# Performance work log

Measured on AMD Instinct MI355X. Metric: run time of the kernel, lower is better.

Reference implementation:

```python
import jax, jax.numpy as jnp
import numpy as np

N_U, N_I, E = 100000, 200000, 500000
CH, H, HD, L, OUT, B_SEED = 128, 4, 32, 2, 64, 1024
NEG_SLOPE = 0.2
LN_EPS = 1e-5


def setup_inputs() -> dict:
    key = jax.random.key(0)
    ks = jax.random.split(key, 24)
    s = 1.0 / np.sqrt(CH)
    inp = {
        'x_user': jax.random.normal(ks[0], (N_U, CH), jnp.float32),
        'x_item': jax.random.normal(ks[1], (N_I, CH), jnp.float32),
        'ui_src': jax.random.randint(ks[2], (E,), 0, N_U, jnp.int32),
        'ui_dst': jax.random.randint(ks[3], (E,), 0, N_I, jnp.int32),
        'iu_src': jax.random.randint(ks[4], (E,), 0, N_I, jnp.int32),
        'iu_dst': jax.random.randint(ks[5], (E,), 0, N_U, jnp.int32),
        'Wsrc_ui': jax.random.normal(ks[6], (L, CH, CH), jnp.float32) * s,
        'Wdst_ui': jax.random.normal(ks[7], (L, CH, CH), jnp.float32) * s,
        'asrc_ui': jax.random.normal(ks[8], (L, H, HD), jnp.float32) * s,
        'adst_ui': jax.random.normal(ks[9], (L, H, HD), jnp.float32) * s,
        'b_ui': jnp.zeros((L, CH), jnp.float32),
        'Wsrc_iu': jax.random.normal(ks[10], (L, CH, CH), jnp.float32) * s,
        'Wdst_iu': jax.random.normal(ks[11], (L, CH, CH), jnp.float32) * s,
        'asrc_iu': jax.random.normal(ks[12], (L, H, HD), jnp.float32) * s,
        'adst_iu': jax.random.normal(ks[13], (L, H, HD), jnp.float32) * s,
        'b_iu': jnp.zeros((L, CH), jnp.float32),
        'ln_w_user': jnp.ones((L, CH), jnp.float32),
        'ln_b_user': jnp.zeros((L, CH), jnp.float32),
        'ln_w_item': jnp.ones((L, CH), jnp.float32),
        'ln_b_item': jnp.zeros((L, CH), jnp.float32),
        'lin_w': jax.random.normal(ks[14], (CH, OUT), jnp.float32) * s,
        'lin_b': jnp.zeros((OUT,), jnp.float32),
        'B': B_SEED,
    }
    return inp


def _gat_conv(x_src, x_dst, src, dst, Ws, Wd, a_s, a_d, b):
    # Bipartite GATConv (PyG semantics, add_self_loops=False, concat=True).
    n_dst = x_dst.shape[0]
    hs = (x_src @ Ws).reshape(-1, H, HD)   # [Ns,H,HD]
    hd = (x_dst @ Wd).reshape(-1, H, HD)   # [Nd,H,HD]
    es = jnp.einsum('nhc,hc->nh', hs, a_s)  # per-node src logits
    ed = jnp.einsum('nhc,hc->nh', hd, a_d)  # per-node dst logits
    e = jax.nn.leaky_relu(es[src] + ed[dst], NEG_SLOPE)  # [E,H]
    # segment softmax over incoming edges of each dst node
    m = jax.ops.segment_max(e, dst, num_segments=n_dst)
    w = jnp.exp(e - m[dst])
    z = jax.ops.segment_sum(w, dst, num_segments=n_dst)
    alpha = w / (z[dst] + 1e-16)
    out = jax.ops.segment_sum(hs[src] * alpha[:, :, None], dst, num_segments=n_dst)
    return out.reshape(n_dst, H * HD) + b


def _layer_norm(x, w, b):
    mu = jnp.mean(x, axis=-1, keepdims=True)
    var = jnp.var(x, axis=-1, keepdims=True)
    return (x - mu) * jax.lax.rsqrt(var + LN_EPS) * w + b


def reference(x_user, x_item, ui_src, ui_dst, iu_src, iu_dst,
              Wsrc_ui, Wdst_ui, asrc_ui, adst_ui, b_ui,
              Wsrc_iu, Wdst_iu, asrc_iu, adst_iu, b_iu,
              ln_w_user, ln_b_user, ln_w_item, ln_b_item,
              lin_w, lin_b, B):
    for l in range(L):
        # HeteroConv with edge_aggr='sum'; each dst node type receives from one edge type here
        xu = _gat_conv(x_item, x_user, iu_src, iu_dst,
                       Wsrc_iu[l], Wdst_iu[l], asrc_iu[l], adst_iu[l], b_iu[l])
        xi = _gat_conv(x_user, x_item, ui_src, ui_dst,
                       Wsrc_ui[l], Wdst_ui[l], asrc_ui[l], adst_ui[l], b_ui[l])
        x_user = jax.nn.relu(_layer_norm(xu, ln_w_user[l], ln_b_user[l]))
        x_item = jax.nn.relu(_layer_norm(xi, ln_w_item[l], ln_b_item[l]))
    return x_user[:B] @ lin_w + lin_b
```

## Files before the change

kernel.cpp:

```cpp
#include <hip/hip_runtime.h>

#define CH 128
#define NHEAD 4

typedef float f32x4 __attribute__((ext_vector_type(4)));
typedef short bf16x8 __attribute__((ext_vector_type(8)));

static __device__ __forceinline__ float b2f(unsigned short u){
  union { unsigned int u; float f; } x; x.u = ((unsigned int)u) << 16; return x.f;
}
static __device__ __forceinline__ unsigned short f2b(float f){
  union { float f; unsigned int u; } x; x.f = f;
  unsigned int r = x.u + 0x7FFFu + ((x.u >> 16) & 1u);
  return (unsigned short)(r >> 16);
}

static __host__ __device__ inline int cdiv_i(int a, int b){ return (a + b - 1) / b; }

__global__ __launch_bounds__(256) void hg_prep0(
    const int* __restrict__ dstU, int* __restrict__ degU,
    const int* __restrict__ dstI, int* __restrict__ degI, int E, int half, int hh,
    const float* __restrict__ xu, unsigned short* __restrict__ yu, long nuv, long nut, int bu,
    const float* __restrict__ xi, unsigned short* __restrict__ yi, long niv, long nit, int bi,
    const float* __restrict__ Wsrc_iu, const float* __restrict__ Wsrc_ui,
    const float* __restrict__ Wdst_iu, const float* __restrict__ Wdst_ui,
    const float* __restrict__ asrc_iu, const float* __restrict__ asrc_ui,
    const float* __restrict__ adst_iu, const float* __restrict__ adst_ui,
    unsigned short* __restrict__ wtAll, float* __restrict__ wdAll, float* __restrict__ wsAll){
  int b = blockIdx.x, tid = threadIdx.x;
  if (b < hh){
    const int* dst; int* deg; int lb;
    if (b < half){ dst = dstU; deg = degU; lb = b; }
    else { dst = dstI; deg = degI; lb = b - half; }
    int t = lb * 256 + tid;
    if (t < E) atomicAdd(&deg[dst[t]], 1);
  } else if (b < hh + bu + bi){
    int cb = b - hh;
    const float* x; unsigned short* y; long nv, nt; int lb;
    if (cb < bu){ x = xu; y = yu; nv = nuv; nt = nut; lb = cb; }
    else { x = xi; y = yi; nv = niv; nt = nit; lb = cb - bu; }
    long t = ((long)lb * 256 + tid) * 4;
    if (t >= nt) return;
    ushort4 o;
    if (t + 3 < nv){
      float4 v = *(const float4*)(x + t);
      o.x = f2b(v.x); o.y = f2b(v.y); o.z = f2b(v.z); o.w = f2b(v.w);
    } else {
      o.x = o.y = o.z = o.w = 0;
    }
    *(ushort4*)(y + t) = o;
  } else {
    int wb = b - hh - bu - bi;
    int ld = wb / 68, r = wb % 68;
    int l = ld >> 1, d = ld & 1;
    const float* Ws = (d ? Wsrc_ui : Wsrc_iu) + (size_t)l*CH*CH;
    const float* Wd = (d ? Wdst_ui : Wdst_iu) + (size_t)l*CH*CH;
    const float* as_ = (d ? asrc_ui : asrc_iu) + (size_t)l*CH;
    const float* ad  = (d ? adst_ui : adst_iu) + (size_t)l*CH;
    unsigned short* wt = wtAll + (size_t)ld*CH*CH;
    float* wd_o = wdAll + (size_t)ld*CH*4;
    float* ws_o = wsAll + (size_t)ld*CH*4;
    if (r < 64){
      int t = r*256 + tid;
      int k = t >> 7, n = t & 127;
      wt[n*CH + k] = f2b(Ws[t]);
    } else if (r < 66){
      int t = (r - 64)*256 + tid;
      int k = t >> 2, h = t & 3;
      float acc = 0.f;
      #pragma unroll 8
      for (int c = 0; c < 32; ++c) acc += Wd[k*CH + h*32 + c] * ad[h*32 + c];
      wd_o[k*4 + h] = acc;
    } else {
      int t = (r - 66)*256 + tid;
      int k = t >> 2, h = t & 3;
      float acc = 0.f;
      #pragma unroll 8
      for (int c = 0; c < 32; ++c) acc += Ws[k*CH + h*32 + c] * as_[h*32 + c];
      ws_o[k*4 + h] = acc;
    }
  }
}

__global__ __launch_bounds__(256) void hg_scan1(const int* __restrict__ degU, int* __restrict__ rpU,
                                                int* __restrict__ bsU, int NU, int nbU,
                                                const int* __restrict__ degI, int* __restrict__ rpI,
                                                int* __restrict__ bsI, int NI){
  __shared__ int sh[256];
  int b = blockIdx.x;
  const int* in; int* out; int* bsums; int N, Ntot, lb;
  if (b < nbU){ in = degU; out = rpU; bsums = bsU; N = NU; Ntot = NU+1; lb = b; }
  else { in = degI; out = rpI; bsums = bsI; N = NI; Ntot = NI+1; lb = b - nbU; }
  int tid = threadIdx.x;
  int base = lb * 2048 + tid * 8;
  int v[8]; int run = 0;
  #pragma unroll
  for (int i = 0; i < 8; ++i){
    int idx = base + i;
    int x = (idx < N) ? in[idx] : 0;
    v[i] = run; run += x;
  }
  sh[tid] = run; __syncthreads();
  #pragma unroll
  for (int off = 1; off < 256; off <<= 1){
    int t = (tid >= off) ? sh[tid - off] : 0;
    __syncthreads();
    sh[tid] += t;
    __syncthreads();
  }
  int excl = tid ? sh[tid-1] : 0;
  #pragma unroll
  for (int i = 0; i < 8; ++i){
    int idx = base + i;
    if (idx < Ntot) out[idx] = excl + v[i];
  }
  if (tid == 255) bsums[lb] = sh[255];
}

__global__ __launch_bounds__(256) void hg_scan2(int* __restrict__ bsU, int nbU,
                                                int* __restrict__ bsI, int nbI){
  __shared__ int sh[256];
  int* bs = (blockIdx.x == 0) ? bsU : bsI;
  int nb  = (blockIdx.x == 0) ? nbU : nbI;
  int t = threadIdx.x;
  sh[t] = (t < nb) ? bs[t] : 0; __syncthreads();
  #pragma unroll
  for (int off = 1; off < 256; off <<= 1){
    int x = (t >= off) ? sh[t - off] : 0;
    __syncthreads();
    sh[t] += x;
    __syncthreads();
  }
  int excl = t ? sh[t-1] : 0;
  if (t < nb) bs[t] = excl;
}

__global__ __launch_bounds__(256) void hg_scan3(int* __restrict__ rpU, const int* __restrict__ bsU,
                                                int* __restrict__ curU, int NtotU, int cU,
                                                int* __restrict__ rpI, const int* __restrict__ bsI,
                                                int* __restrict__ curI, int NtotI){
  int b = blockIdx.x;
  int* out; const int* bsums; int* cursor; int Ntot, lb;
  if (b < cU){ out = rpU; bsums = bsU; cursor = curU; Ntot = NtotU; lb = b; }
  else { out = rpI; bsums = bsI; cursor = curI; Ntot = NtotI; lb = b - cU; }
  int idx = lb * 256 + threadIdx.x;
  if (idx >= Ntot) return;
  int v = out[idx] + bsums[idx >> 11];
  out[idx] = v;
  cursor[idx] = v;
}

__global__ __launch_bounds__(256) void hg_scatter2(const int* __restrict__ dstU, const int* __restrict__ srcU,
                                                   int* __restrict__ curU, int* __restrict__ esU,
                                                   const int* __restrict__ dstI, const int* __restrict__ srcI,
                                                   int* __restrict__ curI, int* __restrict__ esI,
                                                   int E, int half){
  int b = blockIdx.x;
  const int* dst; const int* src; int* cursor; int* esrc; int lb;
  if (b < half){ dst = dstU; src = srcU; cursor = curU; esrc = esU; lb = b; }
  else { dst = dstI; src = srcI; cursor = curI; esrc = esI; lb = b - half; }
  int t = lb * 256 + threadIdx.x;
  if (t >= E) return;
  int d = dst[t];
  int pos = atomicAdd(&cursor[d], 1);
  esrc[pos] = src[t];
}

__global__ __launch_bounds__(256) void hg_gemm2(const unsigned short* __restrict__ X0,
                                                const unsigned short* __restrict__ W0,
                                                unsigned short* __restrict__ Y0, int n0,
                                                const unsigned short* __restrict__ X1,
                                                const unsigned short* __restrict__ W1,
                                                unsigned short* __restrict__ Y1, int n01,
                                                const float* __restrict__ wsU, const float* __restrict__ wdU,
                                                float* __restrict__ esU, float* __restrict__ edU, int NU, int bU,
                                                const float* __restrict__ wsI, const float* __restrict__ wdI,
                                                float* __restrict__ esI, float* __restrict__ edI, int NI){
  __shared__ unsigned short Abuf[CH*CH];
  __shared__ unsigned short Bbuf[CH*CH];
  int tid = threadIdx.x;
  int b = blockIdx.x;

  if (b >= n01){
    int eb = b - n01;
    const unsigned short* x; const float *wsf, *wdf; float *es, *ed; int N, lb;
    if (eb < bU){ x = X1; wsf = wsU; wdf = wdU; es = esU; ed = edU; N = NU; lb = eb; }
    else { x = X0; wsf = wsI; wdf = wdI; es = esI; ed = edI; N = NI; lb = eb - bU; }
    int n = lb * 256 + tid;
    if (n >= N) return;
    const uint4* row = (const uint4*)(x + (size_t)n * CH);
    float s0=0.f,s1=0.f,s2=0.f,s3=0.f,d0=0.f,d1=0.f,d2=0.f,d3=0.f;
    #pragma unroll
    for (int b8 = 0; b8 < 16; ++b8){
      uint4 v = row[b8];
      unsigned int u[4] = {v.x, v.y, v.z, v.w};
      #pragma unroll
      for (int q = 0; q < 4; ++q){
        int k = b8*8 + 2*q;
        float x0 = b2f((unsigned short)(u[q] & 0xffffu));
        float x1 = b2f((unsigned short)(u[q] >> 16));
        float4 a0 = *(const float4*)(wsf + (size_t)k*4);
        float4 a1 = *(const float4*)(wsf + (size_t)(k+1)*4);
        float4 c0 = *(const float4*)(wdf + (size_t)k*4);
        float4 c1 = *(const float4*)(wdf + (size_t)(k+1)*4);
        s0 += x0*a0.x + x1*a1.x;  s1 += x0*a0.y + x1*a1.y;
        s2 += x0*a0.z + x1*a1.z;  s3 += x0*a0.w + x1*a1.w;
        d0 += x0*c0.x + x1*c1.x;  d1 += x0*c0.y + x1*c1.y;
        d2 += x0*c0.z + x1*c1.z;  d3 += x0*c0.w + x1*c1.w;
      }
    }
    float* eo = es + (size_t)n*4;
    eo[0]=s0; eo[1]=s1; eo[2]=s2; eo[3]=s3;
    float* do_ = ed + (size_t)n*4;
    do_[0]=d0; do_[1]=d1; do_[2]=d2; do_[3]=d3;
    return;
  }

  size_t bm = b;
  const unsigned short* X; const unsigned short* W; unsigned short* Y;
  if ((int)bm < n0){ X = X0; W = W0; Y = Y0; }
  else { X = X1; W = W1; Y = Y1; bm -= n0; }
  const unsigned short* xsrc = X + bm * (size_t)(CH*CH);
  #pragma unroll
  for (int it = 0; it < 8; ++it){
    int G = it*256 + tid;
    int m = G >> 4, kg = G & 15;
    int sw = kg ^ (m & 7);
    uint4 va = ((const uint4*)xsrc)[G];
    ((uint4*)Abuf)[m*16 + sw] = va;
    uint4 vb = ((const uint4*)W)[G];
    ((uint4*)Bbuf)[m*16 + sw] = vb;
  }
  __syncthreads();

  int lane = tid & 63, wid = tid >> 6;
  int wr = wid >> 1, wc = wid & 1;
  int l15 = lane & 15, l4 = lane >> 4;
  f32x4 acc[4][4] = {};

  #pragma unroll
  for (int kk = 0; kk < 4; ++kk){
    int kgq = kk*4 + l4;
    bf16x8 af[4], bfr[4];
    #pragma unroll
    for (int i = 0; i < 4; ++i){
      int r = wr*64 + i*16 + l15;
      af[i] = *(const bf16x8*)&Abuf[(r*16 + (kgq ^ (r & 7))) * 8];
      int c = wc*64 + i*16 + l15;
      bfr[i] = *(const bf16x8*)&Bbuf[(c*16 + (kgq ^ (c & 7))) * 8];
    }
    #pragma unroll
    for (int i = 0; i < 4; ++i)
      #pragma unroll
      for (int j = 0; j < 4; ++j)
        acc[i][j] = __builtin_amdgcn_mfma_f32_16x16x32_bf16(af[i], bfr[j], acc[i][j], 0, 0, 0);
  }

  #pragma unroll
  for (int i = 0; i < 4; ++i){
    #pragma unroll
    for (int j = 0; j < 4; ++j){
      int r0 = wr*64 + i*16 + l4*4;
      int c  = wc*64 + j*16 + l15;
      size_t base = (bm*CH + r0) * (size_t)CH + c;
      #pragma unroll
      for (int v = 0; v < 4; ++v)
        Y[base + (size_t)v*CH] = f2b(acc[i][j][v]);
    }
  }
}

#define AGG_ROUND(DEPTH)                                                          \
  for (int j0 = 0; j0 < nb16; j0 += DEPTH){                                       \
    uint4 hv[DEPTH]; float lg[DEPTH];                                             \
    _Pragma("unroll")                                                             \
    for (int k = 0; k < DEPTH; ++k){                                              \
      int jk = j0 + k; jk = (jk < nb16) ? jk : (nb16 - 1);                        \
      int s = __shfl(sj, g*16 + jk);                                              \
      hv[k] = *(const uint4*)(hs + (size_t)s*CH + c16*8);                         \
      lg[k] = eslog[(size_t)s*4 + h];                                             \
    }                                                                             \
    _Pragma("unroll")                                                             \
    for (int k = 0; k < DEPTH; ++k){                                              \
      float ev = lg[k] + edv;                                                     \
      ev = (ev > 0.f) ? ev : 0.2f * ev;                                           \
      float w = ((j0 + k) < nb16) ? __expf(ev) : 0.f;                             \
      zp += w;                                                                    \
      unsigned int u0 = hv[k].x, u1 = hv[k].y, u2 = hv[k].z, u3 = hv[k].w;        \
      pacc[0] += w * b2f((unsigned short)(u0 & 0xffffu));                         \
      pacc[1] += w * b2f((unsigned short)(u0 >> 16));                             \
      pacc[2] += w * b2f((unsigned short)(u1 & 0xffffu));                         \
      pacc[3] += w * b2f((unsigned short)(u1 >> 16));                             \
      pacc[4] += w * b2f((unsigned short)(u2 & 0xffffu));                         \
      pacc[5] += w * b2f((unsigned short)(u2 >> 16));                             \
      pacc[6] += w * b2f((unsigned short)(u3 & 0xffffu));                         \
      pacc[7] += w * b2f((unsigned short)(u3 >> 16));                             \
    }                                                                             \
  }

__global__ __launch_bounds__(256) void hg_agg2(
    const int* __restrict__ rpU, const int* __restrict__ esU,
    const float* __restrict__ eslogU, const float* __restrict__ edU,
    const unsigned short* __restrict__ hsI,
    const float* __restrict__ biasU, const float* __restrict__ lnwU, const float* __restrict__ lnbU,
    unsigned short* __restrict__ xoutU, int NU, int nbU,
    const int* __restrict__ rpI, const int* __restrict__ esI,
    const float* __restrict__ eslogI, const float* __restrict__ edI,
    const unsigned short* __restrict__ hsU,
    const float* __restrict__ biasI, const float* __restrict__ lnwI, const float* __restrict__ lnbI,
    unsigned short* __restrict__ xoutI, int NI){
  int b = blockIdx.x;
  bool isU = (b < nbU);
  const int *rowptr, *esrc; const float *eslog, *ed;
  const unsigned short* hs; const float *bias, *lnw, *lnb;
  unsigned short* xout; int Ndst, lb;
  if (isU){
    rowptr = rpU; esrc = esU; eslog = eslogU; ed = edU; hs = hsI;
    bias = biasU; lnw = lnwU; lnb = lnbU; xout = xoutU; Ndst = NU; lb = b;
  } else {
    rowptr = rpI; esrc = esI; eslog = eslogI; ed = edI; hs = hsU;
    bias = biasI; lnw = lnwI; lnb = lnbI; xout = xoutI; Ndst = NI; lb = b - nbU;
  }
  int tid = threadIdx.x;
  int lane = tid & 63, wid = tid >> 6;
  int g = lane >> 4, c16 = lane & 15, h = c16 >> 2;
  int node = lb * 16 + wid * 4 + g;
  uint4* orow = (uint4*)(xout + (size_t)node * CH);
  if (node >= Ndst){
    uint4 z4 = {0,0,0,0};
    orow[c16] = z4;
    return;
  }

  int begin = rowptr[node], end = rowptr[node + 1];
  int deg = end - begin;
  float edv = ed[(size_t)node*4 + h];
  float pacc[8] = {0.f,0.f,0.f,0.f,0.f,0.f,0.f,0.f};
  float zp = 0.f;

  int nb16 = deg < 16 ? deg : 16;
  int pb = (deg > 0) ? begin : 0;
  int pl = (deg > 0) ? end - 1 : 0;
  int jj = pb + c16; jj = (jj <= pl) ? jj : pl;
  int sj = esrc[jj];

  if (isU){
    AGG_ROUND(8)
  } else {
    AGG_ROUND(4)
  }
  for (int j = begin + 16; j < end; ++j){
    int s = esrc[j];
    float ev = eslog[(size_t)s*4 + h] + edv;
    ev = (ev > 0.f) ? ev : 0.2f * ev;
    float w = __expf(ev);
    zp += w;
    uint4 hv1 = *(const uint4*)(hs + (size_t)s*CH + c16*8);
    unsigned int u[4] = {hv1.x, hv1.y, hv1.z, hv1.w};
    #pragma unroll
    for (int q = 0; q < 4; ++q){
      pacc[2*q]   += w * b2f((unsigned short)(u[q] & 0xffffu));
      pacc[2*q+1] += w * b2f((unsigned short)(u[q] >> 16));
    }
  }

  float rz = (zp > 0.f) ? (1.f / zp) : 0.f;
  float4 b0 = *(const float4*)(bias + c16*8);
  float4 b1 = *(const float4*)(bias + c16*8 + 4);
  float r[8];
  r[0] = pacc[0]*rz + b0.x; r[1] = pacc[1]*rz + b0.y;
  r[2] = pacc[2]*rz + b0.z; r[3] = pacc[3]*rz + b0.w;
  r[4] = pacc[4]*rz + b1.x; r[5] = pacc[5]*rz + b1.y;
  r[6] = pacc[6]*rz + b1.z; r[7] = pacc[7]*rz + b1.w;

  float s1 = 0.f, s2 = 0.f;
  #pragma unroll
  for (int k = 0; k < 8; ++k){ s1 += r[k]; s2 += r[k]*r[k]; }
  #pragma unroll
  for (int off = 1; off < 16; off <<= 1){
    s1 += __shfl_xor(s1, off);
    s2 += __shfl_xor(s2, off);
  }
  float mean = s1 * (1.f/128.f);
  float var  = s2 * (1.f/128.f) - mean*mean;
  float inv  = rsqrtf(var + 1e-5f);

  float4 w0 = *(const float4*)(lnw + c16*8);
  float4 w1 = *(const float4*)(lnw + c16*8 + 4);
  float4 l0 = *(const float4*)(lnb + c16*8);
  float4 l1 = *(const float4*)(lnb + c16*8 + 4);
  float y[8];
  y[0] = (r[0]-mean)*inv*w0.x + l0.x; y[1] = (r[1]-mean)*inv*w0.y + l0.y;
  y[2] = (r[2]-mean)*inv*w0.z + l0.z; y[3] = (r[3]-mean)*inv*w0.w + l0.w;
  y[4] = (r[4]-mean)*inv*w1.x + l1.x; y[5] = (r[5]-mean)*inv*w1.y + l1.y;
  y[6] = (r[6]-mean)*inv*w1.z + l1.z; y[7] = (r[7]-mean)*inv*w1.w + l1.w;
  uint4 o;
  unsigned int* op = (unsigned int*)&o;
  #pragma unroll
  for (int q = 0; q < 4; ++q){
    float a = fmaxf(y[2*q], 0.f), bb = fmaxf(y[2*q+1], 0.f);
    op[q] = (unsigned int)f2b(a) | ((unsigned int)f2b(bb) << 16);
  }
  orow[c16] = o;
}

__global__ __launch_bounds__(256) void hg_final(const unsigned short* __restrict__ x,
                                                const float* __restrict__ w,
                                                const float* __restrict__ b,
                                                float* __restrict__ out, int total, int OUTC){
  int t = blockIdx.x * 256 + threadIdx.x;
  if (t >= total) return;
  int r = t / OUTC, c = t % OUTC;
  const unsigned short* xr = x + (size_t)r * CH;
  float acc = b[c];
  #pragma unroll 8
  for (int k = 0; k < CH; ++k)
    acc += b2f(xr[k]) * w[(size_t)k * OUTC + c];
  out[t] = acc;
}

extern "C" void kernel_launch(void* const* d_in, const int* in_sizes, int n_in,
                              void* d_out, int out_size, void* d_ws, size_t ws_size,
                              hipStream_t stream){
  const float* x_user_f = (const float*)d_in[0];
  const float* x_item_f = (const float*)d_in[1];
  const int* ui_src = (const int*)d_in[2];
  const int* ui_dst = (const int*)d_in[3];
  const int* iu_src = (const int*)d_in[4];
  const int* iu_dst = (const int*)d_in[5];
  const float* Wsrc_ui = (const float*)d_in[6];
  const float* Wdst_ui = (const float*)d_in[7];
  const float* asrc_ui = (const float*)d_in[8];
  const float* adst_ui = (const float*)d_in[9];
  const float* b_ui    = (const float*)d_in[10];
  const float* Wsrc_iu = (const float*)d_in[11];
  const float* Wdst_iu = (const float*)d_in[12];
  const float* asrc_iu = (const float*)d_in[13];
  const float* adst_iu = (const float*)d_in[14];
  const float* b_iu    = (const float*)d_in[15];
  const float* ln_w_user = (const float*)d_in[16];
  const float* ln_b_user = (const float*)d_in[17];
  const float* ln_w_item = (const float*)d_in[18];
  const float* ln_b_item = (const float*)d_in[19];
  const float* lin_w = (const float*)d_in[20];
  const float* lin_b = (const float*)d_in[21];

  const int NU = in_sizes[0] / CH;
  const int NI = in_sizes[1] / CH;
  const int E  = in_sizes[2];
  const int Lnum = in_sizes[6] / (CH*CH);
  const int OUTC = in_sizes[21];
  const int Bn = out_size / OUTC;

  const int NUp = ((NU + 127) / 128) * 128;
  const int NIp = ((NI + 127) / 128) * 128;

  char* ws = (char*)d_ws;
  size_t off = 0;
  auto alloc = [&](size_t bytes)->char*{
    size_t r = (off + 255) & ~(size_t)255;
    off = r + bytes;
    return ws + r;
  };
  unsigned short* xu0 = (unsigned short*)alloc((size_t)NUp * CH * 2);
  unsigned short* xu1 = (unsigned short*)alloc((size_t)NUp * CH * 2);
  unsigned short* xi0 = (unsigned short*)alloc((size_t)NIp * CH * 2);
  unsigned short* xi1 = (unsigned short*)alloc((size_t)NIp * CH * 2);
  unsigned short* hsI = (unsigned short*)alloc((size_t)NIp * CH * 2);
  unsigned short* hsU = (unsigned short*)alloc((size_t)NUp * CH * 2);
  float* esIb = (float*)alloc((size_t)NIp * 4 * 4);
  float* esUb = (float*)alloc((size_t)NUp * 4 * 4);
  float* edU  = (float*)alloc((size_t)NUp * 4 * 4);
  float* edI  = (float*)alloc((size_t)NIp * 4 * 4);
  unsigned short* wtAll = (unsigned short*)alloc((size_t)Lnum * 2 * CH * CH * 2);
  float* wdAll = (float*)alloc((size_t)Lnum * 2 * CH * 4 * 4);
  float* wsAll = (float*)alloc((size_t)Lnum * 2 * CH * 4 * 4);
  int* rowptr_u = (int*)alloc((size_t)(NU + 1) * 4);
  int* cursor_u = (int*)alloc((size_t)(NU + 1) * 4);
  int* rowptr_i = (int*)alloc((size_t)(NI + 1) * 4);
  int* cursor_i = (int*)alloc((size_t)(NI + 1) * 4);
  int* esrc_u = (int*)alloc((size_t)E * 4);
  int* esrc_i = (int*)alloc((size_t)E * 4);
  int* deg    = (int*)alloc((size_t)(NU + NI) * 4);
  int* deg_u  = deg;
  int* deg_i  = deg + NU;
  int* bsums  = (int*)alloc(2048 * 4);
  int* bsU = bsums;
  int* bsI = bsums + 1024;

  hipMemsetAsync(deg, 0, (size_t)(NU + NI) * 4, stream);
  {
    int half = cdiv_i(E, 256), hh = 2*half;
    int bu = cdiv_i(NUp*CH/4, 256), bi = cdiv_i(NIp*CH/4, 256);
    int wp = Lnum*2*68;
    hg_prep0<<<dim3(hh + bu + bi + wp), dim3(256), 0, stream>>>(
        iu_dst, deg_u, ui_dst, deg_i, E, half, hh,
        x_user_f, xu0, (long)NU*CH, (long)NUp*CH, bu,
        x_item_f, xi0, (long)NI*CH, (long)NIp*CH, bi,
        Wsrc_iu, Wsrc_ui, Wdst_iu, Wdst_ui,
        asrc_iu, asrc_ui, adst_iu, adst_ui,
        wtAll, wdAll, wsAll);
  }
  {
    int nbU = cdiv_i(NU + 1, 2048), nbI = cdiv_i(NI + 1, 2048);
    hg_scan1<<<dim3(nbU + nbI), dim3(256), 0, stream>>>(deg_u, rowptr_u, bsU, NU, nbU, deg_i, rowptr_i, bsI, NI);
    hg_scan2<<<dim3(2), dim3(256), 0, stream>>>(bsU, nbU, bsI, nbI);
    int cU = cdiv_i(NU + 1, 256), cI = cdiv_i(NI + 1, 256);
    hg_scan3<<<dim3(cU + cI), dim3(256), 0, stream>>>(rowptr_u, bsU, cursor_u, NU + 1, cU,
                                                      rowptr_i, bsI, cursor_i, NI + 1);
  }
  {
    int half = cdiv_i(E, 256);
    hg_scatter2<<<dim3(2*half), dim3(256), 0, stream>>>(iu_dst, iu_src, cursor_u, esrc_u,
                                                        ui_dst, ui_src, cursor_i, esrc_i, E, half);
  }

  unsigned short *xuA = xu0, *xuB = xu1, *xiA = xi0, *xiB = xi1;
  const int nbkI = NIp/128, nbkU = NUp/128;
  const int bU_esed = cdiv_i(NU, 256), bI_esed = cdiv_i(NI, 256);
  const int aggU = NUp/16, aggI = NIp/16;

  for (int l = 0; l < Lnum; ++l){
    size_t ao = (size_t)l * CH;
    const unsigned short* wtA = wtAll + (size_t)(l*2 + 0) * CH * CH;
    const unsigned short* wtB = wtAll + (size_t)(l*2 + 1) * CH * CH;
    const float* wdA = wdAll + (size_t)(l*2 + 0) * CH * 4;
    const float* wdB = wdAll + (size_t)(l*2 + 1) * CH * 4;
    const float* wsA = wsAll + (size_t)(l*2 + 0) * CH * 4;
    const float* wsB = wsAll + (size_t)(l*2 + 1) * CH * 4;

    hg_gemm2<<<dim3(nbkI + nbkU + bU_esed + bI_esed), dim3(256), 0, stream>>>(
        xiA, wtA, hsI, nbkI,
        xuA, wtB, hsU, nbkI + nbkU,
        wsB, wdA, esUb, edU, NU, bU_esed,
        wsA, wdB, esIb, edI, NI);
    hg_agg2<<<dim3(aggU + aggI), dim3(256), 0, stream>>>(
        rowptr_u, esrc_u, esIb, edU, hsI, b_iu + ao, ln_w_user + ao, ln_b_user + ao, xuB, NU, aggU,
        rowptr_i, esrc_i, esUb, edI, hsU, b_ui + ao, ln_w_item + ao, ln_b_item + ao, xiB, NI);

    unsigned short* t;
    t = xuA; xuA = xuB; xuB = t;
    t = xiA; xiA = xiB; xiB = t;
  }

  hg_final<<<dim3(cdiv_i(Bn*OUTC,256)), dim3(256), 0, stream>>>(xuA, lin_w, lin_b, (float*)d_out, Bn*OUTC, OUTC);
}
```

Baseline: 379.4 us.

## Replace CSR build with fixed-capacity per-node edge buckets plus spill list

Drops the degree-count, three-pass prefix scan and scatter kernels, and instead buckets each edge's source directly into a 16-slot per-destination array using an atomic counter, spilling overflow edges to a global list. Aggregation reads the slot array and, for nodes above capacity, scans the spill list. This removes several launches and passes over the edge arrays during setup, at the cost of more memory and a linear spill scan that would be slow on heavily skewed degree distributions.

Measured after the change: 353.6 us, median of 2. 1.07x faster.

```diff
diff --git a/kernel.cpp b/kernel.cpp
--- a/kernel.cpp
+++ b/kernel.cpp
@@ -2,6 +2,7 @@
 
 #define CH 128
 #define NHEAD 4
+#define CAP 16
 
 typedef float f32x4 __attribute__((ext_vector_type(4)));
 typedef short bf16x8 __attribute__((ext_vector_type(8)));
@@ -17,9 +18,31 @@
 
 static __host__ __device__ inline int cdiv_i(int a, int b){ return (a + b - 1) / b; }
 
-__global__ __launch_bounds__(256) void hg_prep0(
-    const int* __restrict__ dstU, int* __restrict__ degU,
-    const int* __restrict__ dstI, int* __restrict__ degI, int E, int half, int hh,
+__global__ __launch_bounds__(256) void hg_bscat(
+    const int* __restrict__ dstU, const int* __restrict__ srcU,
+    int* __restrict__ cntU, int* __restrict__ slotsU,
+    int* __restrict__ spNU, int* __restrict__ spDU, int* __restrict__ spSU,
+    const int* __restrict__ dstI, const int* __restrict__ srcI,
+    int* __restrict__ cntI, int* __restrict__ slotsI,
+    int* __restrict__ spNI, int* __restrict__ spDI, int* __restrict__ spSI,
+    int E, int half){
+  int b = blockIdx.x;
+  const int *dst, *src; int *cnt, *slots, *spN, *spD, *spS; int lb;
+  if (b < half){ dst=dstU; src=srcU; cnt=cntU; slots=slotsU; spN=spNU; spD=spDU; spS=spSU; lb=b; }
+  else { dst=dstI; src=srcI; cnt=cntI; slots=slotsI; spN=spNI; spD=spDI; spS=spSI; lb=b-half; }
+  int t = lb*256 + threadIdx.x;
+  if (t >= E) return;
+  int d = dst[t], s = src[t];
+  int pos = atomicAdd(&cnt[d], 1);
+  if (pos < CAP){
+    slots[(size_t)d*CAP + pos] = s;
+  } else {
+    int sp = atomicAdd(spN, 1);
+    spD[sp] = d; spS[sp] = s;
+  }
+}
+
+__global__ __launch_bounds__(256) void hg_prep1(
     const float* __restrict__ xu, unsigned short* __restrict__ yu, long nuv, long nut, int bu,
     const float* __restrict__ xi, unsigned short* __restrict__ yi, long niv, long nit, int bi,
     const float* __restrict__ Wsrc_iu, const float* __restrict__ Wsrc_ui,
@@ -28,17 +51,10 @@
     const float* __restrict__ adst_iu, const float* __restrict__ adst_ui,
     unsigned short* __restrict__ wtAll, float* __restrict__ wdAll, float* __restrict__ wsAll){
   int b = blockIdx.x, tid = threadIdx.x;
-  if (b < hh){
-    const int* dst; int* deg; int lb;
-    if (b < half){ dst = dstU; deg = degU; lb = b; }
-    else { dst = dstI; deg = degI; lb = b - half; }
-    int t = lb * 256 + tid;
-    if (t < E) atomicAdd(&deg[dst[t]], 1);
-  } else if (b < hh + bu + bi){
-    int cb = b - hh;
+  if (b < bu + bi){
     const float* x; unsigned short* y; long nv, nt; int lb;
-    if (cb < bu){ x = xu; y = yu; nv = nuv; nt = nut; lb = cb; }
-    else { x = xi; y = yi; nv = niv; nt = nit; lb = cb - bu; }
+    if (b < bu){ x = xu; y = yu; nv = nuv; nt = nut; lb = b; }
+    else { x = xi; y = yi; nv = niv; nt = nit; lb = b - bu; }
     long t = ((long)lb * 256 + tid) * 4;
     if (t >= nt) return;
     ushort4 o;
@@ -50,7 +66,7 @@
     }
     *(ushort4*)(y + t) = o;
   } else {
-    int wb = b - hh - bu - bi;
+    int wb = b - bu - bi;
     int ld = wb / 68, r = wb % 68;
     int l = ld >> 1, d = ld & 1;
     const float* Ws = (d ? Wsrc_ui : Wsrc_iu) + (size_t)l*CH*CH;
@@ -82,90 +98,6 @@
   }
 }
 
-__global__ __launch_bounds__(256) void hg_scan1(const int* __restrict__ degU, int* __restrict__ rpU,
-                                                int* __restrict__ bsU, int NU, int nbU,
-                                                const int* __restrict__ degI, int* __restrict__ rpI,
-                                                int* __restrict__ bsI, int NI){
-  __shared__ int sh[256];
-  int b = blockIdx.x;
-  const int* in; int* out; int* bsums; int N, Ntot, lb;
-  if (b < nbU){ in = degU; out = rpU; bsums = bsU; N = NU; Ntot = NU+1; lb = b; }
-  else { in = degI; out = rpI; bsums = bsI; N = NI; Ntot = NI+1; lb = b - nbU; }
-  int tid = threadIdx.x;
-  int base = lb * 2048 + tid * 8;
-  int v[8]; int run = 0;
-  #pragma unroll
-  for (int i = 0; i < 8; ++i){
-    int idx = base + i;
-    int x = (idx < N) ? in[idx] : 0;
-    v[i] = run; run += x;
-  }
-  sh[tid] = run; __syncthreads();
-  #pragma unroll
-  for (int off = 1; off < 256; off <<= 1){
-    int t = (tid >= off) ? sh[tid - off] : 0;
-    __syncthreads();
-    sh[tid] += t;
-    __syncthreads();
-  }
-  int excl = tid ? sh[tid-1] : 0;
-  #pragma unroll
-  for (int i = 0; i < 8; ++i){
-    int idx = base + i;
-    if (idx < Ntot) out[idx] = excl + v[i];
-  }
-  if (tid == 255) bsums[lb] = sh[255];
-}
-
-__global__ __launch_bounds__(256) void hg_scan2(int* __restrict__ bsU, int nbU,
-                                                int* __restrict__ bsI, int nbI){
-  __shared__ int sh[256];
-  int* bs = (blockIdx.x == 0) ? bsU : bsI;
-  int nb  = (blockIdx.x == 0) ? nbU : nbI;
-  int t = threadIdx.x;
-  sh[t] = (t < nb) ? bs[t] : 0; __syncthreads();
-  #pragma unroll
-  for (int off = 1; off < 256; off <<= 1){
-    int x = (t >= off) ? sh[t - off] : 0;
-    __syncthreads();
-    sh[t] += x;
-    __syncthreads();
-  }
-  int excl = t ? sh[t-1] : 0;
-  if (t < nb) bs[t] = excl;
-}
-
-__global__ __launch_bounds__(256) void hg_scan3(int* __restrict__ rpU, const int* __restrict__ bsU,
-                                                int* __restrict__ curU, int NtotU, int cU,
-                                                int* __restrict__ rpI, const int* __restrict__ bsI,
-                                                int* __restrict__ curI, int NtotI){
-  int b = blockIdx.x;
-  int* out; const int* bsums; int* cursor; int Ntot, lb;
-  if (b < cU){ out = rpU; bsums = bsU; cursor = curU; Ntot = NtotU; lb = b; }
-  else { out = rpI; bsums = bsI; cursor = curI; Ntot = NtotI; lb = b - cU; }
-  int idx = lb * 256 + threadIdx.x;
-  if (idx >= Ntot) return;
-  int v = out[idx] + bsums[idx >> 11];
-  out[idx] = v;
-  cursor[idx] = v;
-}
-
-__global__ __launch_bounds__(256) void hg_scatter2(const int* __restrict__ dstU, const int* __restrict__ srcU,
-                                                   int* __restrict__ curU, int* __restrict__ esU,
-                                                   const int* __restrict__ dstI, const int* __restrict__ srcI,
-                                                   int* __restrict__ curI, int* __restrict__ esI,
-                                                   int E, int half){
-  int b = blockIdx.x;
-  const int* dst; const int* src; int* cursor; int* esrc; int lb;
-  if (b < half){ dst = dstU; src = srcU; cursor = curU; esrc = esU; lb = b; }
-  else { dst = dstI; src = srcI; cursor = curI; esrc = esI; lb = b - half; }
-  int t = lb * 256 + threadIdx.x;
-  if (t >= E) return;
-  int d = dst[t];
-  int pos = atomicAdd(&cursor[d], 1);
-  esrc[pos] = src[t];
-}
-
 __global__ __launch_bounds__(256) void hg_gemm2(const unsigned short* __restrict__ X0,
                                                 const unsigned short* __restrict__ W0,
                                                 unsigned short* __restrict__ Y0, int n0,
@@ -299,26 +231,30 @@
   }
 
 __global__ __launch_bounds__(256) void hg_agg2(
-    const int* __restrict__ rpU, const int* __restrict__ esU,
+    const int* __restrict__ cntU, const int* __restrict__ slotsU,
+    const int* __restrict__ spNU, const int* __restrict__ spDU, const int* __restrict__ spSU,
     const float* __restrict__ eslogU, const float* __restrict__ edU,
     const unsigned short* __restrict__ hsI,
     const float* __restrict__ biasU, const float* __restrict__ lnwU, const float* __restrict__ lnbU,
     unsigned short* __restrict__ xoutU, int NU, int nbU,
-    const int* __restrict__ rpI, const int* __restrict__ esI,
+    const int* __restrict__ cntI, const int* __restrict__ slotsI,
+    const int* __restrict__ spNI, const int* __restrict__ spDI, const int* __restrict__ spSI,
     const float* __restrict__ eslogI, const float* __restrict__ edI,
     const unsigned short* __restrict__ hsU,
     const float* __restrict__ biasI, const float* __restrict__ lnwI, const float* __restrict__ lnbI,
     unsigned short* __restrict__ xoutI, int NI){
   int b = blockIdx.x;
   bool isU = (b < nbU);
-  const int *rowptr, *esrc; const float *eslog, *ed;
+  const int *cnt, *slots, *spN, *spD, *spS; const float *eslog, *ed;
   const unsigned short* hs; const float *bias, *lnw, *lnb;
   unsigned short* xout; int Ndst, lb;
   if (isU){
-    rowptr = rpU; esrc = esU; eslog = eslogU; ed = edU; hs = hsI;
+    cnt = cntU; slots = slotsU; spN = spNU; spD = spDU; spS = spSU;
+    eslog = eslogU; ed = edU; hs = hsI;
     bias = biasU; lnw = lnwU; lnb = lnbU; xout = xoutU; Ndst = NU; lb = b;
   } else {
-    rowptr = rpI; esrc = esI; eslog = eslogI; ed = edI; hs = hsU;
+    cnt = cntI; slots = slotsI; spN = spNI; spD = spDI; spS = spSI;
+    eslog = eslogI; ed = edI; hs = hsU;
     bias = biasI; lnw = lnwI; lnb = lnbI; xout = xoutI; Ndst = NI; lb = b - nbU;
   }
   int tid = threadIdx.x;
@@ -332,35 +268,38 @@
     return;
   }
 
-  int begin = rowptr[node], end = rowptr[node + 1];
-  int deg = end - begin;
+  int deg = cnt[node];
   float edv = ed[(size_t)node*4 + h];
   float pacc[8] = {0.f,0.f,0.f,0.f,0.f,0.f,0.f,0.f};
   float zp = 0.f;
 
-  int nb16 = deg < 16 ? deg : 16;
-  int pb = (deg > 0) ? begin : 0;
-  int pl = (deg > 0) ? end - 1 : 0;
-  int jj = pb + c16; jj = (jj <= pl) ? jj : pl;
-  int sj = esrc[jj];
+  int nb16 = deg < CAP ? deg : CAP;
+  const int* sl = slots + (size_t)node * CAP;
+  int jj = (c16 < nb16) ? c16 : (nb16 > 0 ? nb16 - 1 : 0);
+  int sj = sl[jj];
 
   if (isU){
     AGG_ROUND(8)
   } else {
     AGG_ROUND(4)
   }
-  for (int j = begin + 16; j < end; ++j){
-    int s = esrc[j];
-    float ev = eslog[(size_t)s*4 + h] + edv;
-    ev = (ev > 0.f) ? ev : 0.2f * ev;
-    float w = __expf(ev);
-    zp += w;
-    uint4 hv1 = *(const uint4*)(hs + (size_t)s*CH + c16*8);
-    unsigned int u[4] = {hv1.x, hv1.y, hv1.z, hv1.w};
-    #pragma unroll
-    for (int q = 0; q < 4; ++q){
-      pacc[2*q]   += w * b2f((unsigned short)(u[q] & 0xffffu));
-      pacc[2*q+1] += w * b2f((unsigned short)(u[q] >> 16));
+  if (deg > CAP){
+    int sn = *spN;
+    for (int j = 0; j < sn; ++j){
+      if (spD[j] == node){
+        int s = spS[j];
+        float ev = eslog[(size_t)s*4 + h] + edv;
+        ev = (ev > 0.f) ? ev : 0.2f * ev;
+        float w = __expf(ev);
+        zp += w;
+        uint4 hv1 = *(const uint4*)(hs + (size_t)s*CH + c16*8);
+        unsigned int u[4] = {hv1.x, hv1.y, hv1.z, hv1.w};
+        #pragma unroll
+        for (int q = 0; q < 4; ++q){
+          pacc[2*q]   += w * b2f((unsigned short)(u[q] & 0xffffu));
+          pacc[2*q+1] += w * b2f((unsigned short)(u[q] >> 16));
+        }
+      }
     }
   }
 
@@ -475,44 +414,34 @@
   unsigned short* wtAll = (unsigned short*)alloc((size_t)Lnum * 2 * CH * CH * 2);
   float* wdAll = (float*)alloc((size_t)Lnum * 2 * CH * 4 * 4);
   float* wsAll = (float*)alloc((size_t)Lnum * 2 * CH * 4 * 4);
-  int* rowptr_u = (int*)alloc((size_t)(NU + 1) * 4);
-  int* cursor_u = (int*)alloc((size_t)(NU + 1) * 4);
-  int* rowptr_i = (int*)alloc((size_t)(NI + 1) * 4);
-  int* cursor_i = (int*)alloc((size_t)(NI + 1) * 4);
-  int* esrc_u = (int*)alloc((size_t)E * 4);
-  int* esrc_i = (int*)alloc((size_t)E * 4);
-  int* deg    = (int*)alloc((size_t)(NU + NI) * 4);
-  int* deg_u  = deg;
-  int* deg_i  = deg + NU;
-  int* bsums  = (int*)alloc(2048 * 4);
-  int* bsU = bsums;
-  int* bsI = bsums + 1024;
-
-  hipMemsetAsync(deg, 0, (size_t)(NU + NI) * 4, stream);
+  int* cntAll = (int*)alloc((size_t)(NU + NI + 2) * 4);
+  int* cnt_u = cntAll;
+  int* cnt_i = cntAll + NU;
+  int* spN_u = cntAll + NU + NI;
+  int* spN_i = cntAll + NU + NI + 1;
+  int* slots_u = (int*)alloc((size_t)NU * CAP * 4);
+  int* slots_i = (int*)alloc((size_t)NI * CAP * 4);
+  int* spD_u = (int*)alloc((size_t)E * 4);
+  int* spS_u = (int*)alloc((size_t)E * 4);
+  int* spD_i = (int*)alloc((size_t)E * 4);
+  int* spS_i = (int*)alloc((size_t)E * 4);
+
+  hipMemsetAsync(cntAll, 0, (size_t)(NU + NI + 2) * 4, stream);
   {
-    int half = cdiv_i(E, 256), hh = 2*half;
+    int half = cdiv_i(E, 256);
+    hg_bscat<<<dim3(2*half), dim3(256), 0, stream>>>(
+        iu_dst, iu_src, cnt_u, slots_u, spN_u, spD_u, spS_u,
+        ui_dst, ui_src, cnt_i, slots_i, spN_i, spD_i, spS_i, E, half);
+  }
+  {
     int bu = cdiv_i(NUp*CH/4, 256), bi = cdiv_i(NIp*CH/4, 256);
     int wp = Lnum*2*68;
-    hg_prep0<<<dim3(hh + bu + bi + wp), dim3(256), 0, stream>>>(
-        iu_dst, deg_u, ui_dst, deg_i, E, half, hh,
+    hg_prep1<<<dim3(bu + bi + wp), dim3(256), 0, stream>>>(
         x_user_f, xu0, (long)NU*CH, (long)NUp*CH, bu,
         x_item_f, xi0, (long)NI*CH, (long)NIp*CH, bi,
         Wsrc_iu, Wsrc_ui, Wdst_iu, Wdst_ui,
         asrc_iu, asrc_ui, adst_iu, adst_ui,
         wtAll, wdAll, wsAll);
-  }
-  {
-    int nbU = cdiv_i(NU + 1, 2048), nbI = cdiv_i(NI + 1, 2048);
-    hg_scan1<<<dim3(nbU + nbI), dim3(256), 0, stream>>>(deg_u, rowptr_u, bsU, NU, nbU, deg_i, rowptr_i, bsI, NI);
-    hg_scan2<<<dim3(2), dim3(256), 0, stream>>>(bsU, nbU, bsI, nbI);
-    int cU = cdiv_i(NU + 1, 256), cI = cdiv_i(NI + 1, 256);
-    hg_scan3<<<dim3(cU + cI), dim3(256), 0, stream>>>(rowptr_u, bsU, cursor_u, NU + 1, cU,
-                                                      rowptr_i, bsI, cursor_i, NI + 1);
-  }
-  {
-    int half = cdiv_i(E, 256);
-    hg_scatter2<<<dim3(2*half), dim3(256), 0, stream>>>(iu_dst, iu_src, cursor_u, esrc_u,
-                                                        ui_dst, ui_src, cursor_i, esrc_i, E, half);
   }
 
   unsigned short *xuA = xu0, *xuB = xu1, *xiA = xi0, *xiB = xi1;
@@ -535,8 +464,10 @@
         wsB, wdA, esUb, edU, NU, bU_esed,
         wsA, wdB, esIb, edI, NI);
     hg_agg2<<<dim3(aggU + aggI), dim3(256), 0, stream>>>(
-        rowptr_u, esrc_u, esIb, edU, hsI, b_iu + ao, ln_w_user + ao, ln_b_user + ao, xuB, NU, aggU,
-        rowptr_i, esrc_i, esUb, edI, hsU, b_ui + ao, ln_w_item + ao, ln_b_item + ao, xiB, NI);
+        cnt_u, slots_u, spN_u, spD_u, spS_u, esIb, edU, hsI,
+        b_iu + ao, ln_w_user + ao, ln_b_user + ao, xuB, NU, aggU,
+        cnt_i, slots_i, spN_i, spD_i, spS_i, esUb, edI, hsU,
+        b_ui + ao, ln_w_item + ao, ln_b_item + ao, xiB, NI);
 
     unsigned short* t;
     t = xuA; xuA = xuB; xuB = t;
```
